# Kernel optimization log

Hardware: AMD Instinct MI355X
Metric: run time of the kernel (lower is better)

Reference implementation:

```python
import jax, jax.numpy as jnp
import numpy as np

N, E = 50000, 800000
IN_DIM, HID, OUT = 64, 128, 64
EPS = 1e-5  # BatchNorm eps


def setup_inputs() -> dict:
    key = jax.random.key(0)
    ks = jax.random.split(key, 16)
    def w(k, i, o):
        return jax.random.normal(k, (i, o), jnp.float32) / np.float32(np.sqrt(i))
    def bn(k):
        km, kv = jax.random.split(k)
        return (jnp.ones((HID,), jnp.float32),                       # gamma
                jnp.zeros((HID,), jnp.float32),                      # beta
                0.1 * jax.random.normal(km, (HID,), jnp.float32),    # running mean
                0.5 + jax.random.uniform(kv, (HID,), jnp.float32))   # running var
    g0, be0, m0, v0 = bn(ks[6])
    g1, be1, m1, v1 = bn(ks[7])
    g2, be2, m2, v2 = bn(ks[8])
    return {
        "x":   jax.random.normal(ks[0], (N, IN_DIM), jnp.float32),
        "src": jax.random.randint(ks[1], (E,), 0, N, jnp.int32),
        "dst": jax.random.randint(ks[2], (E,), 0, N, jnp.int32),
        "W0": w(ks[3], IN_DIM, HID), "b0": jnp.zeros((HID,), jnp.float32),
        "g0": g0, "be0": be0, "m0": m0, "v0": v0,
        "W1": w(ks[4], HID, HID), "b1": jnp.zeros((HID,), jnp.float32),
        "g1": g1, "be1": be1, "m1": m1, "v1": v1,
        "W2": w(ks[5], HID, HID), "b2": jnp.zeros((HID,), jnp.float32),
        "g2": g2, "be2": be2, "m2": m2, "v2": v2,
        "Wm1": w(ks[9], HID, HID), "bm1": jnp.zeros((HID,), jnp.float32),
        "Wm2": w(ks[10], HID, OUT), "bm2": jnp.zeros((OUT,), jnp.float32),
    }


def gcn_conv(x, src, dst, W, b):
    # PyG GCNConv: h = x @ W; add self loops; symmetric normalization; scatter-add; + bias
    h = x @ W                                                     # [N, F]
    ones = jnp.ones((src.shape[0],), h.dtype)
    deg = 1.0 + jax.ops.segment_sum(ones, dst, num_segments=N)   # self loop adds 1
    dinv = jax.lax.rsqrt(deg)                                     # deg^-1/2 (deg >= 1)
    coef = (dinv[src] * dinv[dst])[:, None]                       # per-edge norm
    agg = jax.ops.segment_sum(h[src] * coef, dst, num_segments=N)
    return agg + h * (dinv * dinv)[:, None] + b                   # self-loop term + bias


def bn_relu(x, g, be, m, v):
    # eval-mode BatchNorm1d followed by ReLU (dropout is identity in eval)
    return jax.nn.relu((x - m) * jax.lax.rsqrt(v + EPS) * g + be)


def reference(x, src, dst,
              W0, b0, g0, be0, m0, v0,
              W1, b1, g1, be1, m1, v1,
              W2, b2, g2, be2, m2, v2,
              Wm1, bm1, Wm2, bm2):
    h = bn_relu(gcn_conv(x, src, dst, W0, b0), g0, be0, m0, v0)
    h = bn_relu(gcn_conv(h, src, dst, W1, b1), g1, be1, m1, v1)
    h = bn_relu(gcn_conv(h, src, dst, W2, b2), g2, be2, m2, v2)
    h = jax.nn.relu(h @ Wm1 + bm1)
    return h @ Wm2 + bm2
```

## Files before the change

### kernel.cpp

```cpp
#include <hip/hip_runtime.h>
#include <hip/hip_fp16.h>

#define BN_EPS 1e-5f
#define BK 512
#define NBMAX 128
#define ECH 8192
#define BCAP 9216

typedef _Float16 half_t;
typedef _Float16 half8 __attribute__((ext_vector_type(8)));
typedef float floatx4 __attribute__((ext_vector_type(4)));


__global__ __launch_bounds__(256) void scatter_cvt_kernel(
    const int* __restrict__ src, const int* __restrict__ dst,
    int* __restrict__ bcursor, int2* __restrict__ tmp,
    const float* __restrict__ x, __half* __restrict__ x16,
    int E, int nb, int sb, int n4) {
  const int t = threadIdx.x;
  if (blockIdx.x >= sb) {
    int i = (blockIdx.x - sb) * 256 + t;
    if (i < n4) {
      float4 v = *(const float4*)(x + (size_t)i * 4);
      union { __half h[4]; float2 f; } u;
      u.h[0] = __float2half_rn(v.x);
      u.h[1] = __float2half_rn(v.y);
      u.h[2] = __float2half_rn(v.z);
      u.h[3] = __float2half_rn(v.w);
      *(float2*)(x16 + (size_t)i * 4) = u.f;
    }
    return;
  }
  __shared__ int h[NBMAX];
  for (int i = t; i < nb; i += 256) h[i] = 0;
  __syncthreads();
  const int base = blockIdx.x * ECH;
#pragma unroll 8
  for (int p = 0; p < ECH / 256; ++p) {
    int e = base + p * 256 + t;
    if (e < E) atomicAdd(&h[dst[e] >> 9], 1);
  }
  __syncthreads();
  for (int i = t; i < nb; i += 256) {
    int c = h[i];
    h[i] = c ? (i * BCAP + atomicAdd(&bcursor[i], c)) : 0;
  }
  __syncthreads();
#pragma unroll 8
  for (int p = 0; p < ECH / 256; ++p) {
    int e = base + p * 256 + t;
    if (e < E) {
      int s = src[e], d = dst[e];
      int pos = atomicAdd(&h[d >> 9], 1);
      tmp[pos] = make_int2(s, d);
    }
  }
}

__global__ __launch_bounds__(256) void bucket_finalize_kernel(
    const int2* __restrict__ tmp, const int* __restrict__ bcursor,
    int* __restrict__ offs, int* __restrict__ offe, float* __restrict__ dinv,
    int* __restrict__ esrc, int n) {
  __shared__ int deg[BK];
  __shared__ int cur[BK];
  __shared__ int ts[256];
  const int t = threadIdx.x;
  const int b = blockIdx.x;
  const int nbase = b * BK;
  const int nn = min(BK, n - nbase);
  const int cnt = bcursor[b];
  const int2* tp = tmp + (size_t)b * BCAP;
  for (int i = t; i < nn; i += 256) deg[i] = 0;
  __syncthreads();
  for (int e = t; e < cnt; e += 256)
    atomicAdd(&deg[tp[e].y - nbase], 1);
  __syncthreads();
  int d0 = (2 * t < nn) ? deg[2 * t] : 0;
  int d1 = (2 * t + 1 < nn) ? deg[2 * t + 1] : 0;
  ts[t] = d0 + d1;
  __syncthreads();
  for (int o = 1; o < 256; o <<= 1) {
    int v = (t >= o) ? ts[t - o] : 0;
    __syncthreads();
    ts[t] += v;
    __syncthreads();
  }
  int base = b * BCAP + ((t == 0) ? 0 : ts[t - 1]);
  if (2 * t < nn) {
    offs[nbase + 2 * t] = base;
    offe[nbase + 2 * t] = base + d0;
    cur[2 * t] = base;
    dinv[nbase + 2 * t] = rsqrtf(1.0f + (float)d0);
  }
  if (2 * t + 1 < nn) {
    offs[nbase + 2 * t + 1] = base + d0;
    offe[nbase + 2 * t + 1] = base + d0 + d1;
    cur[2 * t + 1] = base + d0;
    dinv[nbase + 2 * t + 1] = rsqrtf(1.0f + (float)d1);
  }
  __syncthreads();
  for (int e = t; e < cnt; e += 256) {
    int2 r = tp[e];
    int pos = atomicAdd(&cur[r.y - nbase], 1);
    esrc[pos] = r.x;
  }
}


template <int FIN, int FOUT, int EPI, bool HALFOUT>
__global__ __launch_bounds__(256) void mgemm_kernel(
    const __half* __restrict__ X, const float* __restrict__ W,
    const float* __restrict__ bias, const float* __restrict__ gam,
    const float* __restrict__ bet, const float* __restrict__ mean,
    const float* __restrict__ var, void* __restrict__ Yv, int n) {
  constexpr int LDK = 72;
  constexpr int NCI = FOUT / 16;
  __shared__ half_t Asm[128 * LDK];
  __shared__ half_t Bsm[FOUT * LDK];

  const int t = threadIdx.x;
  const int wave = t >> 6, lane = t & 63;
  const int quad = lane >> 4, l16 = lane & 15;
  const int rowBase = blockIdx.x * 128;

  floatx4 acc[2][NCI];
#pragma unroll
  for (int i = 0; i < 2; ++i)
#pragma unroll
    for (int ci = 0; ci < NCI; ++ci) acc[i][ci] = (floatx4){0.f, 0.f, 0.f, 0.f};

  for (int kc = 0; kc < FIN; kc += 64) {
    __syncthreads();
    {
      const int kq = t & 15, m0 = t >> 4;
#pragma unroll
      for (int p = 0; p < 8; ++p) {
        int m = p * 16 + m0;
        int row = rowBase + m;
        uint2 v = make_uint2(0u, 0u);
        if (row < n) v = *(const uint2*)(X + (size_t)row * FIN + kc + kq * 4);
        *(uint2*)&Asm[m * LDK + kq * 4] = v;
      }
    }
    {
#pragma unroll
      for (int c0 = 0; c0 < FOUT * 16; c0 += 256) {
        int c = c0 + t;
        int nn = c % FOUT;
        int kg = (c / FOUT) * 4;
        const float* wp = W + (size_t)(kc + kg) * FOUT + nn;
        half_t* d = &Bsm[nn * LDK + kg];
        d[0] = (half_t)wp[0];
        d[1] = (half_t)wp[FOUT];
        d[2] = (half_t)wp[2 * FOUT];
        d[3] = (half_t)wp[3 * FOUT];
      }
    }
    __syncthreads();
#pragma unroll
    for (int kk = 0; kk < 2; ++kk) {
      half8 a0 = *(const half8*)&Asm[(wave * 32 + l16) * LDK + kk * 32 + quad * 8];
      half8 a1 = *(const half8*)&Asm[(wave * 32 + 16 + l16) * LDK + kk * 32 + quad * 8];
#pragma unroll
      for (int ci = 0; ci < NCI; ++ci) {
        half8 b = *(const half8*)&Bsm[(ci * 16 + l16) * LDK + kk * 32 + quad * 8];
        acc[0][ci] = __builtin_amdgcn_mfma_f32_16x16x32_f16(a0, b, acc[0][ci], 0, 0, 0);
        acc[1][ci] = __builtin_amdgcn_mfma_f32_16x16x32_f16(a1, b, acc[1][ci], 0, 0, 0);
      }
    }
  }

  float sc[NCI], sh[NCI];
#pragma unroll
  for (int ci = 0; ci < NCI; ++ci) {
    int col = ci * 16 + l16;
    if constexpr (EPI == 3) {
      float s = gam[col] * rsqrtf(var[col] + BN_EPS);
      sc[ci] = s;
      sh[ci] = (bias[col] - mean[col]) * s + bet[col];
    } else if constexpr (EPI == 1 || EPI == 2) {
      sc[ci] = 1.f;
      sh[ci] = bias[col];
    } else {
      sc[ci] = 1.f;
      sh[ci] = 0.f;
    }
  }
#pragma unroll
  for (int ri = 0; ri < 2; ++ri)
#pragma unroll
    for (int ci = 0; ci < NCI; ++ci) {
      int col = ci * 16 + l16;
#pragma unroll
      for (int r = 0; r < 4; ++r) {
        int row = rowBase + wave * 32 + ri * 16 + quad * 4 + r;
        if (row < n) {
          float v = acc[ri][ci][r];
          if constexpr (EPI != 0) v = fmaf(v, sc[ci], sh[ci]);
          if constexpr (EPI == 1 || EPI == 3) v = fmaxf(v, 0.f);
          if constexpr (HALFOUT)
            ((half_t*)Yv)[(size_t)row * FOUT + col] = (half_t)v;
          else
            ((float*)Yv)[(size_t)row * FOUT + col] = v;
        }
      }
    }
}


__global__ __launch_bounds__(256) void mlp_kernel(
    const __half* __restrict__ X, const float* __restrict__ W1,
    const float* __restrict__ b1f, const float* __restrict__ W2,
    const float* __restrict__ b2f, float* __restrict__ Y, int n) {
  constexpr int LDK = 72;
  constexpr int LDK2 = 136;
  __shared__ half_t smem[(128 + 64) * LDK2];
  half_t* As1 = smem;
  half_t* Bs1 = smem + 128 * LDK;
  half_t* As2 = smem;
  half_t* Bs2 = smem + 128 * LDK2;

  const int t = threadIdx.x;
  const int wave = t >> 6, lane = t & 63;
  const int quad = lane >> 4, l16 = lane & 15;
  const int rowBase = blockIdx.x * 128;

  floatx4 acc[2][8];
#pragma unroll
  for (int i = 0; i < 2; ++i)
#pragma unroll
    for (int ci = 0; ci < 8; ++ci) acc[i][ci] = (floatx4){0.f, 0.f, 0.f, 0.f};

  for (int kc = 0; kc < 128; kc += 64) {
    __syncthreads();
    {
      const int kq = t & 15, m0 = t >> 4;
#pragma unroll
      for (int p = 0; p < 8; ++p) {
        int m = p * 16 + m0;
        int row = rowBase + m;
        uint2 v = make_uint2(0u, 0u);
        if (row < n) v = *(const uint2*)(X + (size_t)row * 128 + kc + kq * 4);
        *(uint2*)&As1[m * LDK + kq * 4] = v;
      }
    }
    {
#pragma unroll
      for (int c0 = 0; c0 < 128 * 16; c0 += 256) {
        int c = c0 + t;
        int nn = c & 127;
        int kg = (c >> 7) << 2;
        const float* wp = W1 + (size_t)(kc + kg) * 128 + nn;
        half_t* d = &Bs1[nn * LDK + kg];
        d[0] = (half_t)wp[0];
        d[1] = (half_t)wp[128];
        d[2] = (half_t)wp[256];
        d[3] = (half_t)wp[384];
      }
    }
    __syncthreads();
#pragma unroll
    for (int kk = 0; kk < 2; ++kk) {
      half8 a0 = *(const half8*)&As1[(wave * 32 + l16) * LDK + kk * 32 + quad * 8];
      half8 a1 = *(const half8*)&As1[(wave * 32 + 16 + l16) * LDK + kk * 32 + quad * 8];
#pragma unroll
      for (int ci = 0; ci < 8; ++ci) {
        half8 b = *(const half8*)&Bs1[(ci * 16 + l16) * LDK + kk * 32 + quad * 8];
        acc[0][ci] = __builtin_amdgcn_mfma_f32_16x16x32_f16(a0, b, acc[0][ci], 0, 0, 0);
        acc[1][ci] = __builtin_amdgcn_mfma_f32_16x16x32_f16(a1, b, acc[1][ci], 0, 0, 0);
      }
    }
  }
  __syncthreads();

#pragma unroll
  for (int ri = 0; ri < 2; ++ri)
#pragma unroll
    for (int ci = 0; ci < 8; ++ci) {
      int col = ci * 16 + l16;
      float bz = b1f[col];
#pragma unroll
      for (int r = 0; r < 4; ++r) {
        int m = wave * 32 + ri * 16 + quad * 4 + r;
        As2[m * LDK2 + col] = (half_t)fmaxf(acc[ri][ci][r] + bz, 0.f);
      }
    }
  {
#pragma unroll
    for (int c0 = 0; c0 < 64 * 32; c0 += 256) {
      int c = c0 + t;
      int nn = c & 63;
      int kg = (c >> 6) << 2;
      const float* wp = W2 + (size_t)kg * 64 + nn;
      half_t* d = &Bs2[nn * LDK2 + kg];
      d[0] = (half_t)wp[0];
      d[1] = (half_t)wp[64];
      d[2] = (half_t)wp[128];
      d[3] = (half_t)wp[192];
    }
  }
  __syncthreads();

  floatx4 acc2[2][4];
#pragma unroll
  for (int i = 0; i < 2; ++i)
#pragma unroll
    for (int ci = 0; ci < 4; ++ci) acc2[i][ci] = (floatx4){0.f, 0.f, 0.f, 0.f};
#pragma unroll
  for (int kk = 0; kk < 4; ++kk) {
    half8 a0 = *(const half8*)&As2[(wave * 32 + l16) * LDK2 + kk * 32 + quad * 8];
    half8 a1 = *(const half8*)&As2[(wave * 32 + 16 + l16) * LDK2 + kk * 32 + quad * 8];
#pragma unroll
    for (int ci = 0; ci < 4; ++ci) {
      half8 b = *(const half8*)&Bs2[(ci * 16 + l16) * LDK2 + kk * 32 + quad * 8];
      acc2[0][ci] = __builtin_amdgcn_mfma_f32_16x16x32_f16(a0, b, acc2[0][ci], 0, 0, 0);
      acc2[1][ci] = __builtin_amdgcn_mfma_f32_16x16x32_f16(a1, b, acc2[1][ci], 0, 0, 0);
    }
  }
#pragma unroll
  for (int ri = 0; ri < 2; ++ri)
#pragma unroll
    for (int ci = 0; ci < 4; ++ci) {
      int col = ci * 16 + l16;
      float bz = b2f[col];
#pragma unroll
      for (int r = 0; r < 4; ++r) {
        int row = rowBase + wave * 32 + ri * 16 + quad * 4 + r;
        if (row < n) Y[(size_t)row * 64 + col] = acc2[ri][ci][r] + bz;
      }
    }
}


__global__ __launch_bounds__(256) void agg64_kernel(
    const __half* __restrict__ h, const int* __restrict__ offs,
    const int* __restrict__ offe, const int* __restrict__ esrc,
    const float* __restrict__ dinv, __half* __restrict__ out, int n) {
  int gi = blockIdx.x * 4 + (threadIdx.x >> 6);
  if (gi >= n) return;
  const int lane = threadIdx.x & 63;
  const float di = dinv[gi];

  float a = 0.f;
  int e = offs[gi];
  const int e1 = offe[gi];
  for (; e + 4 <= e1; e += 4) {
    int s0 = esrc[e], s1 = esrc[e + 1], s2 = esrc[e + 2], s3 = esrc[e + 3];
    float h0 = __half2float(h[((size_t)s0 << 6) + lane]);
    float h1 = __half2float(h[((size_t)s1 << 6) + lane]);
    float h2 = __half2float(h[((size_t)s2 << 6) + lane]);
    float h3 = __half2float(h[((size_t)s3 << 6) + lane]);
    a = fmaf(dinv[s0] * di, h0, a);
    a = fmaf(dinv[s1] * di, h1, a);
    a = fmaf(dinv[s2] * di, h2, a);
    a = fmaf(dinv[s3] * di, h3, a);
  }
  for (; e < e1; ++e) {
    int s = esrc[e];
    a = fmaf(dinv[s] * di, __half2float(h[((size_t)s << 6) + lane]), a);
  }
  a = fmaf(di * di, __half2float(h[((size_t)gi << 6) + lane]), a);
  out[((size_t)gi << 6) + lane] = __float2half_rn(a);
}

__global__ __launch_bounds__(256) void agg128_bn_kernel(
    const __half* __restrict__ h, const int* __restrict__ offs,
    const int* __restrict__ offe, const int* __restrict__ esrc,
    const float* __restrict__ dinv,
    const float* __restrict__ bias, const float* __restrict__ gam,
    const float* __restrict__ bet, const float* __restrict__ mean,
    const float* __restrict__ var, __half* __restrict__ out, int n) {
  int gi = blockIdx.x * 4 + (threadIdx.x >> 6);
  if (gi >= n) return;
  const int lane = threadIdx.x & 63;
  const int c = lane << 1;
  const __half2* hp = (const __half2*)h;
  const float di = dinv[gi];

  float ax = 0.f, ay = 0.f;
  int e = offs[gi];
  const int e1 = offe[gi];
  for (; e + 4 <= e1; e += 4) {
    int s0 = esrc[e], s1 = esrc[e + 1], s2 = esrc[e + 2], s3 = esrc[e + 3];
    float2 h0 = __half22float2(hp[((size_t)s0 << 6) + lane]);
    float2 h1 = __half22float2(hp[((size_t)s1 << 6) + lane]);
    float2 h2 = __half22float2(hp[((size_t)s2 << 6) + lane]);
    float2 h3 = __half22float2(hp[((size_t)s3 << 6) + lane]);
    float c0 = dinv[s0] * di, c1 = dinv[s1] * di;
    float c2 = dinv[s2] * di, c3 = dinv[s3] * di;
    ax = fmaf(c0, h0.x, ax); ay = fmaf(c0, h0.y, ay);
    ax = fmaf(c1, h1.x, ax); ay = fmaf(c1, h1.y, ay);
    ax = fmaf(c2, h2.x, ax); ay = fmaf(c2, h2.y, ay);
    ax = fmaf(c3, h3.x, ax); ay = fmaf(c3, h3.y, ay);
  }
  for (; e < e1; ++e) {
    int s = esrc[e];
    float cf = dinv[s] * di;
    float2 hv = __half22float2(hp[((size_t)s << 6) + lane]);
    ax = fmaf(cf, hv.x, ax);
    ay = fmaf(cf, hv.y, ay);
  }
  float d2 = di * di;
  float2 hs = __half22float2(hp[((size_t)gi << 6) + lane]);
  ax = fmaf(d2, hs.x, ax);
  ay = fmaf(d2, hs.y, ay);

  float2 bv = *(const float2*)(bias + c);
  float2 gv = *(const float2*)(gam + c);
  float2 bev = *(const float2*)(bet + c);
  float2 mv = *(const float2*)(mean + c);
  float2 vv = *(const float2*)(var + c);
  float s0 = gv.x * rsqrtf(vv.x + BN_EPS);
  float s1 = gv.y * rsqrtf(vv.y + BN_EPS);
  float o0 = fmaxf(fmaf(ax + bv.x - mv.x, s0, bev.x), 0.f);
  float o1 = fmaxf(fmaf(ay + bv.y - mv.y, s1, bev.y), 0.f);
  ((__half2*)out)[((size_t)gi << 6) + lane] = __floats2half2_rn(o0, o1);
}


static inline size_t alignup(size_t x, size_t a) { return (x + a - 1) & ~(a - 1); }

extern "C" void kernel_launch(void* const* d_in, const int* in_sizes, int n_in,
                              void* d_out, int out_size, void* d_ws, size_t ws_size,
                              hipStream_t stream) {
  const float* x   = (const float*)d_in[0];
  const int*   src = (const int*)d_in[1];
  const int*   dst = (const int*)d_in[2];
  const float* W0  = (const float*)d_in[3];
  const float* b0  = (const float*)d_in[4];
  const float* g0  = (const float*)d_in[5];
  const float* be0 = (const float*)d_in[6];
  const float* m0  = (const float*)d_in[7];
  const float* v0  = (const float*)d_in[8];
  const float* W1  = (const float*)d_in[9];
  const float* b1  = (const float*)d_in[10];
  const float* g1  = (const float*)d_in[11];
  const float* be1 = (const float*)d_in[12];
  const float* m1  = (const float*)d_in[13];
  const float* v1  = (const float*)d_in[14];
  const float* W2  = (const float*)d_in[15];
  const float* b2  = (const float*)d_in[16];
  const float* g2  = (const float*)d_in[17];
  const float* be2 = (const float*)d_in[18];
  const float* m2  = (const float*)d_in[19];
  const float* v2  = (const float*)d_in[20];
  const float* Wm1 = (const float*)d_in[21];
  const float* bm1 = (const float*)d_in[22];
  const float* Wm2 = (const float*)d_in[23];
  const float* bm2 = (const float*)d_in[24];

  const int N = in_sizes[0] / 64;
  const int E = in_sizes[1];

  char* p = (char*)d_ws;
  auto take = [&](size_t bytes) {
    char* r = p;
    p += alignup(bytes, 256);
    return r;
  };
  const int nbk = (N + BK - 1) / BK;
  int*    bcursor= (int*)take(NBMAX * 4);
  int*    offs   = (int*)take((size_t)N * 4);
  int*    offe   = (int*)take((size_t)N * 4);
  float*  dinv   = (float*)take((size_t)N * 4);
  int*    esrc   = (int*)take((size_t)nbk * BCAP * 4);
  int2*   tmp    = (int2*)take((size_t)nbk * BCAP * 8);
  __half* x16    = (__half*)take((size_t)N * 64 * 2);
  __half* aggx16 = (__half*)take((size_t)N * 64 * 2);
  __half* t0     = (__half*)take((size_t)N * 128 * 2);
  __half* t1     = (__half*)take((size_t)N * 128 * 2);
  float*  yout   = (float*)d_out;

  const int TB = 256;
  const int sb = (E + ECH - 1) / ECH;
  const int n4 = N * 16;
  const int cb = (n4 + 255) / 256;

  hipMemsetAsync(bcursor, 0, NBMAX * 4, stream);
  scatter_cvt_kernel<<<sb + cb, TB, 0, stream>>>(src, dst, bcursor, tmp,
                                                 x, x16, E, nbk, sb, n4);
  bucket_finalize_kernel<<<nbk, TB, 0, stream>>>(tmp, bcursor, offs, offe,
                                                 dinv, esrc, N);

  const int gemmGrid = (N + 127) / 128;
  const int aggGrid = (N + 3) / 4;

  agg64_kernel<<<aggGrid, TB, 0, stream>>>(x16, offs, offe, esrc, dinv, aggx16, N);
  mgemm_kernel<64, 128, 3, true><<<gemmGrid, TB, 0, stream>>>(
      aggx16, W0, b0, g0, be0, m0, v0, t0, N);
  mgemm_kernel<128, 128, 0, true><<<gemmGrid, TB, 0, stream>>>(
      t0, W1, nullptr, nullptr, nullptr, nullptr, nullptr, t1, N);
  agg128_bn_kernel<<<aggGrid, TB, 0, stream>>>(t1, offs, offe, esrc, dinv,
                                               b1, g1, be1, m1, v1, t0, N);
  mgemm_kernel<128, 128, 0, true><<<gemmGrid, TB, 0, stream>>>(
      t0, W2, nullptr, nullptr, nullptr, nullptr, nullptr, t1, N);
  agg128_bn_kernel<<<aggGrid, TB, 0, stream>>>(t1, offs, offe, esrc, dinv,
                                               b2, g2, be2, m2, v2, t0, N);
  mlp_kernel<<<gemmGrid, TB, 0, stream>>>(t0, Wm1, bm1, Wm2, bm2, yout, N);
}
```

Before: 321.3 us.

## Slice aggregation by feature columns and prescale GEMM rows by dinv

```diff
diff --git a/kernel.cpp b/kernel.cpp
--- a/kernel.cpp
+++ b/kernel.cpp
@@ -186,6 +186,16 @@
       sh[ci] = 0.f;
     }
   }
+  float rs[2][4];
+  if constexpr (EPI == 4) {
+#pragma unroll
+    for (int ri = 0; ri < 2; ++ri)
+#pragma unroll
+      for (int r = 0; r < 4; ++r) {
+        int row = rowBase + wave * 32 + ri * 16 + quad * 4 + r;
+        rs[ri][r] = (row < n) ? bias[row] : 0.f;
+      }
+  }
 #pragma unroll
   for (int ri = 0; ri < 2; ++ri)
 #pragma unroll
@@ -196,7 +206,8 @@
         int row = rowBase + wave * 32 + ri * 16 + quad * 4 + r;
         if (row < n) {
           float v = acc[ri][ci][r];
-          if constexpr (EPI != 0) v = fmaf(v, sc[ci], sh[ci]);
+          if constexpr (EPI == 4) v *= rs[ri][r];
+          if constexpr (EPI == 1 || EPI == 2 || EPI == 3) v = fmaf(v, sc[ci], sh[ci]);
           if constexpr (EPI == 1 || EPI == 3) v = fmaxf(v, 0.f);
           if constexpr (HALFOUT)
             ((half_t*)Yv)[(size_t)row * FOUT + col] = (half_t)v;
@@ -332,89 +343,113 @@
 }
 
 
-__global__ __launch_bounds__(256) void agg64_kernel(
+__global__ __launch_bounds__(256) void agg64_slice_kernel(
     const __half* __restrict__ h, const int* __restrict__ offs,
     const int* __restrict__ offe, const int* __restrict__ esrc,
-    const float* __restrict__ dinv, __half* __restrict__ out, int n) {
-  int gi = blockIdx.x * 4 + (threadIdx.x >> 6);
+    const float* __restrict__ dinv, __half* __restrict__ out,
+    int n, int nchunk) {
+  const int b = blockIdx.x;
+  const int x = b & 7;
+  const int slice = x & 1;
+  const int chunk = (b >> 3) * 4 + (x >> 1);
+  if (chunk >= nchunk) return;
+  const int gi = chunk * 4 + (threadIdx.x >> 6);
   if (gi >= n) return;
   const int lane = threadIdx.x & 63;
+  const int grp = lane >> 4;
+  const int fo = slice * 16 + (lane & 15);
+  const __half2* hp = (const __half2*)h;
   const float di = dinv[gi];
 
-  float a = 0.f;
-  int e = offs[gi];
+  float ax = 0.f, ay = 0.f, bx = 0.f, by = 0.f;
+  int e = offs[gi] + grp;
   const int e1 = offe[gi];
-  for (; e + 4 <= e1; e += 4) {
-    int s0 = esrc[e], s1 = esrc[e + 1], s2 = esrc[e + 2], s3 = esrc[e + 3];
-    float h0 = __half2float(h[((size_t)s0 << 6) + lane]);
-    float h1 = __half2float(h[((size_t)s1 << 6) + lane]);
-    float h2 = __half2float(h[((size_t)s2 << 6) + lane]);
-    float h3 = __half2float(h[((size_t)s3 << 6) + lane]);
-    a = fmaf(dinv[s0] * di, h0, a);
-    a = fmaf(dinv[s1] * di, h1, a);
-    a = fmaf(dinv[s2] * di, h2, a);
-    a = fmaf(dinv[s3] * di, h3, a);
-  }
-  for (; e < e1; ++e) {
-    int s = esrc[e];
-    a = fmaf(dinv[s] * di, __half2float(h[((size_t)s << 6) + lane]), a);
-  }
-  a = fmaf(di * di, __half2float(h[((size_t)gi << 6) + lane]), a);
-  out[((size_t)gi << 6) + lane] = __float2half_rn(a);
-}
-
-__global__ __launch_bounds__(256) void agg128_bn_kernel(
+  for (; e + 4 < e1; e += 8) {
+    int s0 = __builtin_nontemporal_load(esrc + e);
+    int s1 = __builtin_nontemporal_load(esrc + e + 4);
+    float c0 = dinv[s0] * di, c1 = dinv[s1] * di;
+    float2 h0 = __half22float2(hp[((size_t)s0 << 5) + fo]);
+    float2 h1 = __half22float2(hp[((size_t)s1 << 5) + fo]);
+    ax = fmaf(c0, h0.x, ax); ay = fmaf(c0, h0.y, ay);
+    bx = fmaf(c1, h1.x, bx); by = fmaf(c1, h1.y, by);
+  }
+  if (e < e1) {
+    int s = __builtin_nontemporal_load(esrc + e);
+    float cf = dinv[s] * di;
+    float2 hv = __half22float2(hp[((size_t)s << 5) + fo]);
+    ax = fmaf(cf, hv.x, ax); ay = fmaf(cf, hv.y, ay);
+  }
+  ax += bx; ay += by;
+  ax += __shfl_down(ax, 32); ay += __shfl_down(ay, 32);
+  ax += __shfl_down(ax, 16); ay += __shfl_down(ay, 16);
+  if (grp == 0) {
+    float d2 = di * di;
+    float2 hs = __half22float2(hp[((size_t)gi << 5) + fo]);
+    ax = fmaf(d2, hs.x, ax); ay = fmaf(d2, hs.y, ay);
+    __half2 o2 = __floats2half2_rn(ax, ay);
+    __builtin_nontemporal_store(*(unsigned int*)&o2,
+        (unsigned int*)((__half2*)out + (((size_t)gi << 5) + fo)));
+  }
+}
+
+__global__ __launch_bounds__(256) void agg128_bn_slice_kernel(
     const __half* __restrict__ h, const int* __restrict__ offs,
     const int* __restrict__ offe, const int* __restrict__ esrc,
     const float* __restrict__ dinv,
     const float* __restrict__ bias, const float* __restrict__ gam,
     const float* __restrict__ bet, const float* __restrict__ mean,
-    const float* __restrict__ var, __half* __restrict__ out, int n) {
-  int gi = blockIdx.x * 4 + (threadIdx.x >> 6);
+    const float* __restrict__ var, __half* __restrict__ out,
+    int n, int nchunk) {
+  const int b = blockIdx.x;
+  const int x = b & 7;
+  const int slice = x & 3;
+  const int chunk = (b >> 3) * 2 + (x >> 2);
+  if (chunk >= nchunk) return;
+  const int gi = chunk * 4 + (threadIdx.x >> 6);
   if (gi >= n) return;
   const int lane = threadIdx.x & 63;
-  const int c = lane << 1;
+  const int grp = lane >> 4;
+  const int fo = slice * 16 + (lane & 15);
   const __half2* hp = (const __half2*)h;
   const float di = dinv[gi];
 
-  float ax = 0.f, ay = 0.f;
-  int e = offs[gi];
+  float ax = 0.f, ay = 0.f, bx = 0.f, by = 0.f;
+  int e = offs[gi] + grp;
   const int e1 = offe[gi];
-  for (; e + 4 <= e1; e += 4) {
-    int s0 = esrc[e], s1 = esrc[e + 1], s2 = esrc[e + 2], s3 = esrc[e + 3];
-    float2 h0 = __half22float2(hp[((size_t)s0 << 6) + lane]);
-    float2 h1 = __half22float2(hp[((size_t)s1 << 6) + lane]);
-    float2 h2 = __half22float2(hp[((size_t)s2 << 6) + lane]);
-    float2 h3 = __half22float2(hp[((size_t)s3 << 6) + lane]);
-    float c0 = dinv[s0] * di, c1 = dinv[s1] * di;
-    float c2 = dinv[s2] * di, c3 = dinv[s3] * di;
-    ax = fmaf(c0, h0.x, ax); ay = fmaf(c0, h0.y, ay);
-    ax = fmaf(c1, h1.x, ax); ay = fmaf(c1, h1.y, ay);
-    ax = fmaf(c2, h2.x, ax); ay = fmaf(c2, h2.y, ay);
-    ax = fmaf(c3, h3.x, ax); ay = fmaf(c3, h3.y, ay);
-  }
-  for (; e < e1; ++e) {
-    int s = esrc[e];
-    float cf = dinv[s] * di;
-    float2 hv = __half22float2(hp[((size_t)s << 6) + lane]);
-    ax = fmaf(cf, hv.x, ax);
-    ay = fmaf(cf, hv.y, ay);
-  }
-  float d2 = di * di;
-  float2 hs = __half22float2(hp[((size_t)gi << 6) + lane]);
-  ax = fmaf(d2, hs.x, ax);
-  ay = fmaf(d2, hs.y, ay);
-
-  float2 bv = *(const float2*)(bias + c);
-  float2 gv = *(const float2*)(gam + c);
-  float2 bev = *(const float2*)(bet + c);
-  float2 mv = *(const float2*)(mean + c);
-  float2 vv = *(const float2*)(var + c);
-  float s0 = gv.x * rsqrtf(vv.x + BN_EPS);
-  float s1 = gv.y * rsqrtf(vv.y + BN_EPS);
-  float o0 = fmaxf(fmaf(ax + bv.x - mv.x, s0, bev.x), 0.f);
-  float o1 = fmaxf(fmaf(ay + bv.y - mv.y, s1, bev.y), 0.f);
-  ((__half2*)out)[((size_t)gi << 6) + lane] = __floats2half2_rn(o0, o1);
+  for (; e + 4 < e1; e += 8) {
+    int s0 = __builtin_nontemporal_load(esrc + e);
+    int s1 = __builtin_nontemporal_load(esrc + e + 4);
+    float2 h0 = __half22float2(hp[((size_t)s0 << 6) + fo]);
+    float2 h1 = __half22float2(hp[((size_t)s1 << 6) + fo]);
+    ax += h0.x; ay += h0.y;
+    bx += h1.x; by += h1.y;
+  }
+  if (e < e1) {
+    int s = __builtin_nontemporal_load(esrc + e);
+    float2 hv = __half22float2(hp[((size_t)s << 6) + fo]);
+    ax += hv.x; ay += hv.y;
+  }
+  ax += bx; ay += by;
+  ax += __shfl_down(ax, 32); ay += __shfl_down(ay, 32);
+  ax += __shfl_down(ax, 16); ay += __shfl_down(ay, 16);
+  if (grp == 0) {
+    float2 hs = __half22float2(hp[((size_t)gi << 6) + fo]);
+    ax = di * (ax + hs.x);
+    ay = di * (ay + hs.y);
+    int c = fo << 1;
+    float2 bv = *(const float2*)(bias + c);
+    float2 gv = *(const float2*)(gam + c);
+    float2 bev = *(const float2*)(bet + c);
+    float2 mv = *(const float2*)(mean + c);
+    float2 vv = *(const float2*)(var + c);
+    float s0 = gv.x * rsqrtf(vv.x + BN_EPS);
+    float s1 = gv.y * rsqrtf(vv.y + BN_EPS);
+    float o0 = fmaxf(fmaf(ax + bv.x - mv.x, s0, bev.x), 0.f);
+    float o1 = fmaxf(fmaf(ay + bv.y - mv.y, s1, bev.y), 0.f);
+    __half2 o2 = __floats2half2_rn(o0, o1);
+    __builtin_nontemporal_store(*(unsigned int*)&o2,
+        (unsigned int*)((__half2*)out + (((size_t)gi << 6) + fo)));
+  }
 }
 
 
@@ -483,18 +518,21 @@
                                                  dinv, esrc, N);
 
   const int gemmGrid = (N + 127) / 128;
-  const int aggGrid = (N + 3) / 4;
-
-  agg64_kernel<<<aggGrid, TB, 0, stream>>>(x16, offs, offe, esrc, dinv, aggx16, N);
+  const int nchunk = (N + 3) / 4;
+  const int g64grid = 8 * ((nchunk + 3) / 4);
+  const int g128grid = 8 * ((nchunk + 1) / 2);
+
+  agg64_slice_kernel<<<g64grid, TB, 0, stream>>>(x16, offs, offe, esrc, dinv,
+                                                 aggx16, N, nchunk);
   mgemm_kernel<64, 128, 3, true><<<gemmGrid, TB, 0, stream>>>(
       aggx16, W0, b0, g0, be0, m0, v0, t0, N);
-  mgemm_kernel<128, 128, 0, true><<<gemmGrid, TB, 0, stream>>>(
-      t0, W1, nullptr, nullptr, nullptr, nullptr, nullptr, t1, N);
-  agg128_bn_kernel<<<aggGrid, TB, 0, stream>>>(t1, offs, offe, esrc, dinv,
-                                               b1, g1, be1, m1, v1, t0, N);
-  mgemm_kernel<128, 128, 0, true><<<gemmGrid, TB, 0, stream>>>(
-      t0, W2, nullptr, nullptr, nullptr, nullptr, nullptr, t1, N);
-  agg128_bn_kernel<<<aggGrid, TB, 0, stream>>>(t1, offs, offe, esrc, dinv,
-                                               b2, g2, be2, m2, v2, t0, N);
+  mgemm_kernel<128, 128, 4, true><<<gemmGrid, TB, 0, stream>>>(
+      t0, W1, dinv, nullptr, nullptr, nullptr, nullptr, t1, N);
+  agg128_bn_slice_kernel<<<g128grid, TB, 0, stream>>>(t1, offs, offe, esrc, dinv,
+                                                      b1, g1, be1, m1, v1, t0, N, nchunk);
+  mgemm_kernel<128, 128, 4, true><<<gemmGrid, TB, 0, stream>>>(
+      t0, W2, dinv, nullptr, nullptr, nullptr, nullptr, t1, N);
+  agg128_bn_slice_kernel<<<g128grid, TB, 0, stream>>>(t1, offs, offe, esrc, dinv,
+                                                      b2, g2, be2, m2, v2, t0, N, nchunk);
   mlp_kernel<<<gemmGrid, TB, 0, stream>>>(t0, Wm1, bm1, Wm2, bm2, yout, N);
 }
```

Measured after the change: 491.5 us. 1.53x slower.

## Pre-scale features by dinv so aggregation gathers skip per-edge dinv loads

Applied to the files above, without the earlier changes.

```diff
diff --git a/kernel.cpp b/kernel.cpp
--- a/kernel.cpp
+++ b/kernel.cpp
@@ -60,9 +60,10 @@
 __global__ __launch_bounds__(256) void bucket_finalize_kernel(
     const int2* __restrict__ tmp, const int* __restrict__ bcursor,
     int* __restrict__ offs, int* __restrict__ offe, float* __restrict__ dinv,
-    int* __restrict__ esrc, int n) {
+    int* __restrict__ esrc, __half* __restrict__ x16, int n) {
   __shared__ int deg[BK];
   __shared__ int cur[BK];
+  __shared__ float fdi[BK];
   __shared__ int ts[256];
   const int t = threadIdx.x;
   const int b = blockIdx.x;
@@ -87,22 +88,34 @@
   }
   int base = b * BCAP + ((t == 0) ? 0 : ts[t - 1]);
   if (2 * t < nn) {
+    float di = rsqrtf(1.0f + (float)d0);
     offs[nbase + 2 * t] = base;
     offe[nbase + 2 * t] = base + d0;
     cur[2 * t] = base;
-    dinv[nbase + 2 * t] = rsqrtf(1.0f + (float)d0);
+    fdi[2 * t] = di;
+    dinv[nbase + 2 * t] = di;
   }
   if (2 * t + 1 < nn) {
+    float di = rsqrtf(1.0f + (float)d1);
     offs[nbase + 2 * t + 1] = base + d0;
     offe[nbase + 2 * t + 1] = base + d0 + d1;
     cur[2 * t + 1] = base + d0;
-    dinv[nbase + 2 * t + 1] = rsqrtf(1.0f + (float)d1);
+    fdi[2 * t + 1] = di;
+    dinv[nbase + 2 * t + 1] = di;
   }
   __syncthreads();
   for (int e = t; e < cnt; e += 256) {
     int2 r = tp[e];
     int pos = atomicAdd(&cur[r.y - nbase], 1);
     esrc[pos] = r.x;
+  }
+  __half2* xp = (__half2*)x16;
+  for (int i = t; i < nn * 32; i += 256) {
+    int nl = i >> 5;
+    size_t idx = (((size_t)(nbase + nl)) << 5) + (i & 31);
+    float2 v = __half22float2(xp[idx]);
+    float s = fdi[nl];
+    xp[idx] = __floats2half2_rn(v.x * s, v.y * s);
   }
 }
 
@@ -186,6 +199,16 @@
       sh[ci] = 0.f;
     }
   }
+  float rs[2][4];
+  if constexpr (EPI == 4) {
+#pragma unroll
+    for (int ri = 0; ri < 2; ++ri)
+#pragma unroll
+      for (int r = 0; r < 4; ++r) {
+        int row = rowBase + wave * 32 + ri * 16 + quad * 4 + r;
+        rs[ri][r] = (row < n) ? bias[row] : 0.f;
+      }
+  }
 #pragma unroll
   for (int ri = 0; ri < 2; ++ri)
 #pragma unroll
@@ -196,7 +219,8 @@
         int row = rowBase + wave * 32 + ri * 16 + quad * 4 + r;
         if (row < n) {
           float v = acc[ri][ci][r];
-          if constexpr (EPI != 0) v = fmaf(v, sc[ci], sh[ci]);
+          if constexpr (EPI == 4) v *= rs[ri][r];
+          if constexpr (EPI == 1 || EPI == 2 || EPI == 3) v = fmaf(v, sc[ci], sh[ci]);
           if constexpr (EPI == 1 || EPI == 3) v = fmaxf(v, 0.f);
           if constexpr (HALFOUT)
             ((half_t*)Yv)[(size_t)row * FOUT + col] = (half_t)v;
@@ -341,26 +365,30 @@
   const int lane = threadIdx.x & 63;
   const float di = dinv[gi];
 
-  float a = 0.f;
+  float a0 = 0.f, a1 = 0.f, a2 = 0.f, a3 = 0.f;
   int e = offs[gi];
   const int e1 = offe[gi];
-  for (; e + 4 <= e1; e += 4) {
-    int s0 = esrc[e], s1 = esrc[e + 1], s2 = esrc[e + 2], s3 = esrc[e + 3];
+  for (; e + 8 <= e1; e += 8) {
+    int s0 = esrc[e],     s1 = esrc[e + 1], s2 = esrc[e + 2], s3 = esrc[e + 3];
+    int s4 = esrc[e + 4], s5 = esrc[e + 5], s6 = esrc[e + 6], s7 = esrc[e + 7];
     float h0 = __half2float(h[((size_t)s0 << 6) + lane]);
     float h1 = __half2float(h[((size_t)s1 << 6) + lane]);
     float h2 = __half2float(h[((size_t)s2 << 6) + lane]);
     float h3 = __half2float(h[((size_t)s3 << 6) + lane]);
-    a = fmaf(dinv[s0] * di, h0, a);
-    a = fmaf(dinv[s1] * di, h1, a);
-    a = fmaf(dinv[s2] * di, h2, a);
-    a = fmaf(dinv[s3] * di, h3, a);
+    float h4 = __half2float(h[((size_t)s4 << 6) + lane]);
+    float h5 = __half2float(h[((size_t)s5 << 6) + lane]);
+    float h6 = __half2float(h[((size_t)s6 << 6) + lane]);
+    float h7 = __half2float(h[((size_t)s7 << 6) + lane]);
+    a0 += h0; a1 += h1; a2 += h2; a3 += h3;
+    a0 += h4; a1 += h5; a2 += h6; a3 += h7;
   }
   for (; e < e1; ++e) {
     int s = esrc[e];
-    a = fmaf(dinv[s] * di, __half2float(h[((size_t)s << 6) + lane]), a);
-  }
-  a = fmaf(di * di, __half2float(h[((size_t)gi << 6) + lane]), a);
-  out[((size_t)gi << 6) + lane] = __float2half_rn(a);
+    a0 += __half2float(h[((size_t)s << 6) + lane]);
+  }
+  float a = (a0 + a1) + (a2 + a3);
+  a += __half2float(h[((size_t)gi << 6) + lane]);
+  out[((size_t)gi << 6) + lane] = __float2half_rn(di * a);
 }
 
 __global__ __launch_bounds__(256) void agg128_bn_kernel(
@@ -377,33 +405,37 @@
   const __half2* hp = (const __half2*)h;
   const float di = dinv[gi];
 
-  float ax = 0.f, ay = 0.f;
+  float ax = 0.f, ay = 0.f, bx = 0.f, by = 0.f;
+  float cx = 0.f, cy = 0.f, dx = 0.f, dy = 0.f;
   int e = offs[gi];
   const int e1 = offe[gi];
-  for (; e + 4 <= e1; e += 4) {
-    int s0 = esrc[e], s1 = esrc[e + 1], s2 = esrc[e + 2], s3 = esrc[e + 3];
+  for (; e + 8 <= e1; e += 8) {
+    int s0 = esrc[e],     s1 = esrc[e + 1], s2 = esrc[e + 2], s3 = esrc[e + 3];
+    int s4 = esrc[e + 4], s5 = esrc[e + 5], s6 = esrc[e + 6], s7 = esrc[e + 7];
     float2 h0 = __half22float2(hp[((size_t)s0 << 6) + lane]);
     float2 h1 = __half22float2(hp[((size_t)s1 << 6) + lane]);
     float2 h2 = __half22float2(hp[((size_t)s2 << 6) + lane]);
     float2 h3 = __half22float2(hp[((size_t)s3 << 6) + lane]);
-    float c0 = dinv[s0] * di, c1 = dinv[s1] * di;
-    float c2 = dinv[s2] * di, c3 = dinv[s3] * di;
-    ax = fmaf(c0, h0.x, ax); ay = fmaf(c0, h0.y, ay);
-    ax = fmaf(c1, h1.x, ax); ay = fmaf(c1, h1.y, ay);
-    ax = fmaf(c2, h2.x, ax); ay = fmaf(c2, h2.y, ay);
-    ax = fmaf(c3, h3.x, ax); ay = fmaf(c3, h3.y, ay);
+    float2 h4 = __half22float2(hp[((size_t)s4 << 6) + lane]);
+    float2 h5 = __half22float2(hp[((size_t)s5 << 6) + lane]);
+    float2 h6 = __half22float2(hp[((size_t)s6 << 6) + lane]);
+    float2 h7 = __half22float2(hp[((size_t)s7 << 6) + lane]);
+    ax += h0.x; ay += h0.y; bx += h1.x; by += h1.y;
+    cx += h2.x; cy += h2.y; dx += h3.x; dy += h3.y;
+    ax += h4.x; ay += h4.y; bx += h5.x; by += h5.y;
+    cx += h6.x; cy += h6.y; dx += h7.x; dy += h7.y;
   }
   for (; e < e1; ++e) {
     int s = esrc[e];
-    float cf = dinv[s] * di;
     float2 hv = __half22float2(hp[((size_t)s << 6) + lane]);
-    ax = fmaf(cf, hv.x, ax);
-    ay = fmaf(cf, hv.y, ay);
-  }
-  float d2 = di * di;
+    ax += hv.x;
+    ay += hv.y;
+  }
+  ax = (ax + bx) + (cx + dx);
+  ay = (ay + by) + (cy + dy);
   float2 hs = __half22float2(hp[((size_t)gi << 6) + lane]);
-  ax = fmaf(d2, hs.x, ax);
-  ay = fmaf(d2, hs.y, ay);
+  ax = di * (ax + hs.x);
+  ay = di * (ay + hs.y);
 
   float2 bv = *(const float2*)(bias + c);
   float2 gv = *(const float2*)(gam + c);
@@ -480,7 +512,7 @@
   scatter_cvt_kernel<<<sb + cb, TB, 0, stream>>>(src, dst, bcursor, tmp,
                                                  x, x16, E, nbk, sb, n4);
   bucket_finalize_kernel<<<nbk, TB, 0, stream>>>(tmp, bcursor, offs, offe,
-                                                 dinv, esrc, N);
+                                                 dinv, esrc, x16, N);
 
   const int gemmGrid = (N + 127) / 128;
   const int aggGrid = (N + 3) / 4;
@@ -488,12 +520,12 @@
   agg64_kernel<<<aggGrid, TB, 0, stream>>>(x16, offs, offe, esrc, dinv, aggx16, N);
   mgemm_kernel<64, 128, 3, true><<<gemmGrid, TB, 0, stream>>>(
       aggx16, W0, b0, g0, be0, m0, v0, t0, N);
-  mgemm_kernel<128, 128, 0, true><<<gemmGrid, TB, 0, stream>>>(
-      t0, W1, nullptr, nullptr, nullptr, nullptr, nullptr, t1, N);
+  mgemm_kernel<128, 128, 4, true><<<gemmGrid, TB, 0, stream>>>(
+      t0, W1, dinv, nullptr, nullptr, nullptr, nullptr, t1, N);
   agg128_bn_kernel<<<aggGrid, TB, 0, stream>>>(t1, offs, offe, esrc, dinv,
                                                b1, g1, be1, m1, v1, t0, N);
-  mgemm_kernel<128, 128, 0, true><<<gemmGrid, TB, 0, stream>>>(
-      t0, W2, nullptr, nullptr, nullptr, nullptr, nullptr, t1, N);
+  mgemm_kernel<128, 128, 4, true><<<gemmGrid, TB, 0, stream>>>(
+      t0, W2, dinv, nullptr, nullptr, nullptr, nullptr, t1, N);
   agg128_bn_kernel<<<aggGrid, TB, 0, stream>>>(t1, offs, offe, esrc, dinv,
                                                b2, g2, be2, m2, v2, t0, N);
   mlp_kernel<<<gemmGrid, TB, 0, stream>>>(t0, Wm1, bm1, Wm2, bm2, yout, N);
```

New measurement: 346.7 us. 7.9% more time.
